# Optimization experiments

Measured on AMD Instinct MI355X. Metric: run time of the kernel, lower is better.

The kernel has to match this reference:

```python
import jax, jax.numpy as jnp
import numpy as np

K_DIM = 256
HEADS = 8


def setup_inputs() -> dict:
    key = jax.random.key(0)
    ks = jax.random.split(key, 6)
    b, t, k, h = 8, 1024, K_DIM, HEADS
    scale = 1.0 / np.sqrt(k)
    x = jax.random.normal(ks[0], (b, t, k), dtype=jnp.float32)
    # nn.Linear(k, k*h, bias=False) weights, stored as (in, out) for x @ W
    Wq = jax.random.normal(ks[1], (k, k * h), dtype=jnp.float32) * scale
    Wk = jax.random.normal(ks[2], (k, k * h), dtype=jnp.float32) * scale
    Wv = jax.random.normal(ks[3], (k, k * h), dtype=jnp.float32) * scale
    # unifyheads: nn.Linear(h*k, k) with bias
    Wu = jax.random.normal(ks[4], (h * k, k), dtype=jnp.float32) * (1.0 / np.sqrt(h * k))
    bu = jax.random.normal(ks[5], (k,), dtype=jnp.float32) * 0.01
    return {"x": x, "Wq": Wq, "Wk": Wk, "Wv": Wv, "Wu": Wu, "bu": bu}


def reference(x, Wq, Wk, Wv, Wu, bu):
    b, t, k = x.shape
    h = Wq.shape[1] // k
    inv4 = 1.0 / (k ** 0.25)  # scale Q and K each by k^(1/4) -> combined 1/sqrt(k)
    q = (x @ Wq).reshape(b, t, h, k) * inv4
    kk = (x @ Wk).reshape(b, t, h, k) * inv4
    v = (x @ Wv).reshape(b, t, h, k)
    # scores: [b, h, t, t]
    scores = jnp.einsum('bthk,bshk->bhts', q, kk)
    att = jax.nn.softmax(scores, axis=-1)
    out = jnp.einsum('bhts,bshk->bthk', att, v).reshape(b, t, h * k)
    return out @ Wu + bu
```

## Files before the change

### kernel.cpp

```cpp
#include <hip/hip_runtime.h>
#include <stdint.h>

typedef unsigned short u16;
typedef __attribute__((ext_vector_type(8))) short bf16x8;
typedef __attribute__((ext_vector_type(4))) float f32x4;

#define LOG2E 1.44269504088896340736f

__device__ __forceinline__ float bf2f(u16 u) {
  union { uint32_t u; float f; } v; v.u = ((uint32_t)u) << 16; return v.f;
}
__device__ __forceinline__ u16 f2bf(float f) {
  union { float f; uint32_t u; } v; v.f = f;
  uint32_t r = v.u + 0x7fffu + ((v.u >> 16) & 1u);
  return (u16)(r >> 16);
}

__device__ __forceinline__ void gl_lds16(const u16* g, u16* l) {
  __builtin_amdgcn_global_load_lds((const __attribute__((address_space(1))) void*)g,
                                   (__attribute__((address_space(3))) void*)l, 16, 0, 0);
}

__global__ __launch_bounds__(256) void k_cvt_x(const float* __restrict__ x,
                                               u16* __restrict__ xb) {
  const int i = blockIdx.x * 256 + threadIdx.x;
  float4 v = ((const float4*)x)[i];
  ushort4 o;
  o.x = f2bf(v.x); o.y = f2bf(v.y); o.z = f2bf(v.z); o.w = f2bf(v.w);
  ((ushort4*)xb)[i] = o;
}

__device__ __forceinline__ void transpose64f(const float* src, int sstride,
                                             u16* dst, int dstride,
                                             float scale, u16* tile ) {
  const int tid = threadIdx.x;
  const int row = tid >> 3, seg = tid & 7;
#pragma unroll
  for (int p = 0; p < 2; ++p) {
    int rr = p * 32 + row;
    int rw = rr ^ (seg * 8);
    float4 a = *(const float4*)(src + rr * sstride + seg * 8);
    float4 b = *(const float4*)(src + rr * sstride + seg * 8 + 4);
    tile[(seg * 8 + 0) * 80 + rw] = f2bf(a.x * scale);
    tile[(seg * 8 + 1) * 80 + rw] = f2bf(a.y * scale);
    tile[(seg * 8 + 2) * 80 + rw] = f2bf(a.z * scale);
    tile[(seg * 8 + 3) * 80 + rw] = f2bf(a.w * scale);
    tile[(seg * 8 + 4) * 80 + rw] = f2bf(b.x * scale);
    tile[(seg * 8 + 5) * 80 + rw] = f2bf(b.y * scale);
    tile[(seg * 8 + 6) * 80 + rw] = f2bf(b.z * scale);
    tile[(seg * 8 + 7) * 80 + rw] = f2bf(b.w * scale);
  }
  __syncthreads();
#pragma unroll
  for (int p = 0; p < 2; ++p) {
    int rr = p * 32 + row;
    int sw = (seg ^ ((rr >> 3) & 7)) * 8;
    *(uint4*)(dst + rr * dstride + seg * 8) = *(uint4*)(tile + rr * 80 + sw);
  }
}

__device__ __forceinline__ void transpose64(const u16* src, int sstride,
                                            u16* dst, int dstride, u16* tile) {
  const int tid = threadIdx.x;
  const int row = tid >> 3, seg = tid & 7;
  union { uint4 u; u16 s[8]; } tv;
#pragma unroll
  for (int p = 0; p < 2; ++p) {
    int rr = p * 32 + row;
    int rw = rr ^ (seg * 8);
    tv.u = *(const uint4*)(src + rr * sstride + seg * 8);
#pragma unroll
    for (int j = 0; j < 8; ++j)
      tile[(seg * 8 + j) * 80 + rw] = tv.s[j];
  }
  __syncthreads();
#pragma unroll
  for (int p = 0; p < 2; ++p) {
    int rr = p * 32 + row;
    int sw = (seg ^ ((rr >> 3) & 7)) * 8;
    *(uint4*)(dst + rr * dstride + seg * 8) = *(uint4*)(tile + rr * 80 + sw);
  }
}

__global__ __launch_bounds__(256) void k_transpose_wqkv(const float* __restrict__ Wq,
                                                        const float* __restrict__ Wk,
                                                        const float* __restrict__ Wv,
                                                        u16* __restrict__ Wt) {
  __shared__ u16 tile[64 * 80];
  const int o0 = blockIdx.x * 64, i0 = blockIdx.y * 64;
  const float* src; float scale = 0.25f; int oc0 = o0;
  if (o0 < 2048)      { src = Wq; }
  else if (o0 < 4096) { src = Wk; oc0 = o0 - 2048; }
  else                { src = Wv; oc0 = o0 - 4096; scale = 1.0f; }
  transpose64f(src + i0 * 2048 + oc0, 2048, Wt + o0 * 256 + i0, 256, scale, tile);
}

__global__ __launch_bounds__(256) void k_transpose_wu(const float* __restrict__ Wu,
                                                      u16* __restrict__ Wut) {
  __shared__ u16 tile[64 * 80];
  const int c0 = blockIdx.x * 64, r0 = blockIdx.y * 64;
  transpose64f(Wu + r0 * 256 + c0, 256, Wut + c0 * 2048 + r0, 2048, 1.0f, tile);
}

__global__ __launch_bounds__(256) void k_transpose_v(const u16* __restrict__ qkv,
                                                     u16* __restrict__ vt) {
  __shared__ u16 tile[64 * 80];
  const int bh = blockIdx.z;
  const int b = bh >> 3, h = bh & 7;
  const int t0 = blockIdx.y * 64, d0 = blockIdx.x * 64;
  const u16* src = qkv + ((size_t)(b * 1024 + t0)) * 6144 + 4096 + h * 256 + d0;
  u16* dst = vt + ((size_t)(bh * 256 + d0)) * 1024 + t0;
  transpose64(src, 6144, dst, 1024, tile);
}

__global__ __launch_bounds__(256) void k_gemm_qkv(const u16* __restrict__ A,
                                                  const u16* __restrict__ Bt,
                                                  u16* __restrict__ C) {
  __shared__ u16 As[128 * 32];
  __shared__ u16 Bs[128 * 32];
  const int m0 = blockIdx.y * 128, n0 = blockIdx.x * 128;
  const int tid = threadIdx.x, w = tid >> 6, lane = tid & 63;
  const int q = lane >> 4, r = lane & 15;
  const int wm = (w >> 1) * 64, wn = (w & 1) * 64;
  const int bo0 = w * 2048 + lane * 16;
  const int row0 = bo0 >> 6, col0 = (bo0 & 63) >> 1;
  const int bo1 = bo0 + 1024;
  const int row1 = bo1 >> 6, col1 = (bo1 & 63) >> 1;
  f32x4 acc[4][4] = {};
  for (int kt = 0; kt < 256; kt += 32) {
    __syncthreads();
    gl_lds16(A + (m0 + row0) * 256 + kt + col0, As + w * 1024);
    gl_lds16(A + (m0 + row1) * 256 + kt + col1, As + w * 1024 + 512);
    gl_lds16(Bt + (n0 + row0) * 256 + kt + col0, Bs + w * 1024);
    gl_lds16(Bt + (n0 + row1) * 256 + kt + col1, Bs + w * 1024 + 512);
    __syncthreads();
    bf16x8 af[4], bf[4];
#pragma unroll
    for (int mb = 0; mb < 4; ++mb) af[mb] = *(const bf16x8*)(As + (wm + mb * 16 + r) * 32 + q * 8);
#pragma unroll
    for (int nb = 0; nb < 4; ++nb) bf[nb] = *(const bf16x8*)(Bs + (wn + nb * 16 + r) * 32 + q * 8);
#pragma unroll
    for (int mb = 0; mb < 4; ++mb)
#pragma unroll
      for (int nb = 0; nb < 4; ++nb)
        acc[mb][nb] = __builtin_amdgcn_mfma_f32_16x16x32_bf16(af[mb], bf[nb], acc[mb][nb], 0, 0, 0);
  }
#pragma unroll
  for (int mb = 0; mb < 4; ++mb)
#pragma unroll
    for (int nb = 0; nb < 4; ++nb) {
      const int nn = n0 + wn + nb * 16 + r;
#pragma unroll
      for (int reg = 0; reg < 4; ++reg) {
        const int mm = m0 + wm + mb * 16 + q * 4 + reg;
        C[(size_t)mm * 6144 + nn] = f2bf(acc[mb][nb][reg]);
      }
    }
}

__global__ __launch_bounds__(256) void k_attn(const u16* __restrict__ qkv,
                                              const u16* __restrict__ vt,
                                              u16* __restrict__ att) {
  __shared__ u16 smem[16896];
  const int blk = blockIdx.x;
  const int qt = blk >> 6, bh = blk & 63;
  const int b = bh >> 3, h = bh & 7;
  const int tid = threadIdx.x, w = tid >> 6, lane = tid & 63;
  const int q = lane >> 4, r = lane & 15;
  const int t0 = qt * 64 + w * 16;

  const u16* Qg = qkv + ((size_t)(b * 1024 + t0 + r)) * 6144 + h * 256;
  bf16x8 qf[8];
#pragma unroll
  for (int kc = 0; kc < 8; ++kc) qf[kc] = *(const bf16x8*)(Qg + kc * 32 + q * 8);

  float m_i = -3.0e38f, l_i = 0.0f;
  f32x4 o[16] = {};

  const u16* Kg = qkv + (size_t)b * 1024 * 6144 + 2048 + h * 256;
  const u16* Vg = vt + (size_t)(b * 8 + h) * 256 * 1024;

  const int kc_s = (tid & 31) >> 2, kq_s = tid & 3;
  const int db_s = tid >> 4, vr_s = tid & 15;

  for (int sc = 0; sc < 1024; sc += 32) {
    __syncthreads();
    {
      uint4 kv[4];
#pragma unroll
      for (int p = 0; p < 4; ++p) {
        int key = p * 8 + (tid >> 5);
        kv[p] = *(const uint4*)(Kg + (size_t)(sc + key) * 6144 + (tid & 31) * 8);
      }
#pragma unroll
      for (int p = 0; p < 4; ++p) {
        int key = p * 8 + (tid >> 5);
        int sb = key >> 4, kr = key & 15;
        int unit = (kc_s * 2 + sb) * 64 + kq_s * 16 + ((kr + kq_s) & 15);
        *(uint4*)(smem + unit * 8) = kv[p];
      }
    }
    {
      uint4 vv[4];
#pragma unroll
      for (int p = 0; p < 4; ++p)
        vv[p] = *(const uint4*)(Vg + (size_t)tid * 1024 + sc + p * 8);
#pragma unroll
      for (int p = 0; p < 4; ++p) {
        int unit = db_s * 64 + p * 16 + ((vr_s + p) & 15);
        *(uint4*)(smem + 8192 + unit * 8) = vv[p];
      }
    }
    __syncthreads();

    f32x4 s0 = {}, s1 = {};
#pragma unroll
    for (int kc = 0; kc < 8; ++kc) {
      bf16x8 k0 = *(const bf16x8*)(smem + ((kc * 2 + 0) * 64 + q * 16 + ((r + q) & 15)) * 8);
      bf16x8 k1 = *(const bf16x8*)(smem + ((kc * 2 + 1) * 64 + q * 16 + ((r + q) & 15)) * 8);
      s0 = __builtin_amdgcn_mfma_f32_16x16x32_bf16(k0, qf[kc], s0, 0, 0, 0);
      s1 = __builtin_amdgcn_mfma_f32_16x16x32_bf16(k1, qf[kc], s1, 0, 0, 0);
    }

    float vmax = fmaxf(fmaxf(fmaxf(s0[0], s0[1]), fmaxf(s0[2], s0[3])),
                       fmaxf(fmaxf(s1[0], s1[1]), fmaxf(s1[2], s1[3])));
    vmax = fmaxf(vmax, __shfl_xor(vmax, 16));
    vmax = fmaxf(vmax, __shfl_xor(vmax, 32));
    float mn = fmaxf(m_i, vmax);
    float al = exp2f((m_i - mn) * LOG2E);
    float pa[4], pb[4];
    float rs = 0.0f;
#pragma unroll
    for (int reg = 0; reg < 4; ++reg) {
      pa[reg] = exp2f((s0[reg] - mn) * LOG2E);
      pb[reg] = exp2f((s1[reg] - mn) * LOG2E);
      rs += pa[reg] + pb[reg];
    }
    rs += __shfl_xor(rs, 16);
    rs += __shfl_xor(rs, 32);
    l_i = l_i * al + rs;
    m_i = mn;
    if (__any(al < 0.99999f)) {
#pragma unroll
      for (int db = 0; db < 16; ++db) {
        f32x4 t = o[db];
#pragma unroll
        for (int reg = 0; reg < 4; ++reg) t[reg] *= al;
        o[db] = t;
      }
    }

    uint32_t pk[4];
#pragma unroll
    for (int reg = 0; reg < 4; ++reg)
      pk[reg] = (uint32_t)f2bf(pa[reg]) | ((uint32_t)f2bf(pb[reg]) << 16);
    const int srcA = ((q & 1) << 5) + r;
    const int srcB = srcA + 16;
    uint32_t tt[8];
#pragma unroll
    for (int reg = 0; reg < 4; ++reg) tt[reg] = (uint32_t)__shfl((int)pk[reg], srcA);
#pragma unroll
    for (int reg = 0; reg < 4; ++reg) tt[4 + reg] = (uint32_t)__shfl((int)pk[reg], srcB);
    union { bf16x8 v; u16 e[8]; } pf;
    const bool hi = (q >= 2);
#pragma unroll
    for (int j = 0; j < 8; ++j)
      pf.e[j] = hi ? (u16)(tt[j] >> 16) : (u16)(tt[j] & 0xffffu);

#pragma unroll
    for (int db = 0; db < 16; ++db) {
      bf16x8 vf = *(const bf16x8*)(smem + 8192 + (db * 64 + q * 16 + ((r + q) & 15)) * 8);
      o[db] = __builtin_amdgcn_mfma_f32_16x16x32_bf16(vf, pf.v, o[db], 0, 0, 0);
    }
  }

  float rl = 1.0f / l_i;
  __syncthreads();
  u16* Os = smem + w * 4224;
#pragma unroll
  for (int db = 0; db < 16; ++db) {
    uint32_t lo = (uint32_t)f2bf(o[db][0] * rl) | ((uint32_t)f2bf(o[db][1] * rl) << 16);
    uint32_t hi2 = (uint32_t)f2bf(o[db][2] * rl) | ((uint32_t)f2bf(o[db][3] * rl) << 16);
    uint2 val; val.x = lo; val.y = hi2;
    *(uint2*)(Os + r * 264 + db * 16 + q * 4) = val;
  }
  asm volatile("s_waitcnt lgkmcnt(0)" ::: "memory");
  u16* Ag = att + ((size_t)(b * 1024 + t0)) * 2048 + h * 256;
#pragma unroll
  for (int p = 0; p < 8; ++p) {
    int idx = (p * 64 + lane) * 8;
    int row = idx >> 8, col = idx & 255;
    *(uint4*)(Ag + (size_t)row * 2048 + col) = *(uint4*)(Os + row * 264 + col);
  }
}

__global__ __launch_bounds__(256) void k_gemm_out(const u16* __restrict__ A,
                                                  const u16* __restrict__ Bt,
                                                  const float* __restrict__ bu,
                                                  float* __restrict__ C) {
  __shared__ u16 As[128 * 32];
  __shared__ u16 Bs[64 * 32];
  const int m0 = blockIdx.y * 128, n0 = blockIdx.x * 64;
  const int tid = threadIdx.x, w = tid >> 6, lane = tid & 63;
  const int q = lane >> 4, r = lane & 15;
  const int wm = (w >> 1) * 64, wn = (w & 1) * 32;
  const int boA0 = w * 2048 + lane * 16;
  const int rA0 = boA0 >> 6, cA0 = (boA0 & 63) >> 1;
  const int boA1 = boA0 + 1024;
  const int rA1 = boA1 >> 6, cA1 = (boA1 & 63) >> 1;
  const int boB = w * 1024 + lane * 16;
  const int rB = boB >> 6, cB = (boB & 63) >> 1;
  f32x4 acc[4][2] = {};
  for (int kt = 0; kt < 2048; kt += 32) {
    __syncthreads();
    gl_lds16(A + (size_t)(m0 + rA0) * 2048 + kt + cA0, As + w * 1024);
    gl_lds16(A + (size_t)(m0 + rA1) * 2048 + kt + cA1, As + w * 1024 + 512);
    gl_lds16(Bt + (size_t)(n0 + rB) * 2048 + kt + cB, Bs + w * 512);
    __syncthreads();
    bf16x8 af[4], bf[2];
#pragma unroll
    for (int mb = 0; mb < 4; ++mb) af[mb] = *(const bf16x8*)(As + (wm + mb * 16 + r) * 32 + q * 8);
#pragma unroll
    for (int nb = 0; nb < 2; ++nb) bf[nb] = *(const bf16x8*)(Bs + (wn + nb * 16 + r) * 32 + q * 8);
#pragma unroll
    for (int mb = 0; mb < 4; ++mb)
#pragma unroll
      for (int nb = 0; nb < 2; ++nb)
        acc[mb][nb] = __builtin_amdgcn_mfma_f32_16x16x32_bf16(af[mb], bf[nb], acc[mb][nb], 0, 0, 0);
  }
  float bias[2];
#pragma unroll
  for (int nb = 0; nb < 2; ++nb) bias[nb] = bu[n0 + wn + nb * 16 + r];
#pragma unroll
  for (int mb = 0; mb < 4; ++mb)
#pragma unroll
    for (int nb = 0; nb < 2; ++nb) {
      const int nn = n0 + wn + nb * 16 + r;
#pragma unroll
      for (int reg = 0; reg < 4; ++reg) {
        const int mm = m0 + wm + mb * 16 + q * 4 + reg;
        C[(size_t)mm * 256 + nn] = acc[mb][nb][reg] + bias[nb];
      }
    }
}

extern "C" void kernel_launch(void* const* d_in, const int* in_sizes, int n_in,
                              void* d_out, int out_size, void* d_ws, size_t ws_size,
                              hipStream_t stream) {
  const float* x  = (const float*)d_in[0];
  const float* Wq = (const float*)d_in[1];
  const float* Wk = (const float*)d_in[2];
  const float* Wv = (const float*)d_in[3];
  const float* Wu = (const float*)d_in[4];
  const float* bu = (const float*)d_in[5];
  float* outp = (float*)d_out;

  char* ws = (char*)d_ws;
  u16* qkv   = (u16*)(ws);
  u16* vt    = (u16*)(ws + 100663296);
  u16* attb  = (u16*)(ws + 134217728);
  u16* wqkvt = (u16*)(ws + 167772160);
  u16* wut   = (u16*)(ws + 170917888);
  u16* xb    = (u16*)(ws + 171966464);
  (void)in_sizes; (void)n_in; (void)out_size; (void)ws_size;

  dim3 blk(256);
  k_cvt_x<<<dim3(2048), blk, 0, stream>>>(x, xb);
  k_transpose_wqkv<<<dim3(96, 4), blk, 0, stream>>>(Wq, Wk, Wv, wqkvt);
  k_transpose_wu<<<dim3(4, 32), blk, 0, stream>>>(Wu, wut);
  k_gemm_qkv<<<dim3(48, 64), blk, 0, stream>>>(xb, wqkvt, qkv);
  k_transpose_v<<<dim3(4, 16, 64), blk, 0, stream>>>(qkv, vt);
  k_attn<<<dim3(1024), blk, 0, stream>>>(qkv, vt, attb);
  k_gemm_out<<<dim3(4, 64), blk, 0, stream>>>(attb, wut, bu, outp);
}
```

Baseline: 323.1 us.

## Process two 16-row query tiles per wave in attention kernel

Each wave now handles 32 query rows (two independent 16-row tiles) instead of 16, so every K/V tile staged in shared memory feeds twice as many MFMAs. The grid is halved to 512 blocks of 128 queries each, which halves the global-to-LDS traffic for K and V per query. In exchange, register pressure roughly doubles (two output accumulator sets of 16 f32x4), and there are fewer blocks to spread across the GPU's compute units. The launch bound now requests 2 blocks per SIMD.

```diff
diff --git a/kernel.cpp b/kernel.cpp
--- a/kernel.cpp
+++ b/kernel.cpp
@@ -158,24 +158,28 @@
     }
 }
 
-__global__ __launch_bounds__(256) void k_attn(const u16* __restrict__ qkv,
-                                              const u16* __restrict__ vt,
-                                              u16* __restrict__ att) {
+__global__ __launch_bounds__(256, 2) void k_attn(const u16* __restrict__ qkv,
+                                                 const u16* __restrict__ vt,
+                                                 u16* __restrict__ att) {
   __shared__ u16 smem[16896];
   const int blk = blockIdx.x;
   const int qt = blk >> 6, bh = blk & 63;
   const int b = bh >> 3, h = bh & 7;
   const int tid = threadIdx.x, w = tid >> 6, lane = tid & 63;
   const int q = lane >> 4, r = lane & 15;
-  const int t0 = qt * 64 + w * 16;
-
-  const u16* Qg = qkv + ((size_t)(b * 1024 + t0 + r)) * 6144 + h * 256;
-  bf16x8 qf[8];
-#pragma unroll
-  for (int kc = 0; kc < 8; ++kc) qf[kc] = *(const bf16x8*)(Qg + kc * 32 + q * 8);
-
-  float m_i = -3.0e38f, l_i = 0.0f;
-  f32x4 o[16] = {};
+  const int t0 = qt * 128 + w * 32;
+
+  const u16* QgA = qkv + ((size_t)(b * 1024 + t0 + r)) * 6144 + h * 256;
+  const u16* QgB = QgA + (size_t)16 * 6144;
+  bf16x8 qfA[8], qfB[8];
+#pragma unroll
+  for (int kc = 0; kc < 8; ++kc) {
+    qfA[kc] = *(const bf16x8*)(QgA + kc * 32 + q * 8);
+    qfB[kc] = *(const bf16x8*)(QgB + kc * 32 + q * 8);
+  }
+
+  float mA = -3.0e38f, lA = 0.0f, mB = -3.0e38f, lB = 0.0f;
+  f32x4 oA[16] = {}, oB[16] = {};
 
   const u16* Kg = qkv + (size_t)b * 1024 * 6144 + 2048 + h * 256;
   const u16* Vg = vt + (size_t)(b * 8 + h) * 256 * 1024;
@@ -213,84 +217,133 @@
     }
     __syncthreads();
 
-    f32x4 s0 = {}, s1 = {};
+    f32x4 s0A = {}, s1A = {}, s0B = {}, s1B = {};
 #pragma unroll
     for (int kc = 0; kc < 8; ++kc) {
       bf16x8 k0 = *(const bf16x8*)(smem + ((kc * 2 + 0) * 64 + q * 16 + ((r + q) & 15)) * 8);
       bf16x8 k1 = *(const bf16x8*)(smem + ((kc * 2 + 1) * 64 + q * 16 + ((r + q) & 15)) * 8);
-      s0 = __builtin_amdgcn_mfma_f32_16x16x32_bf16(k0, qf[kc], s0, 0, 0, 0);
-      s1 = __builtin_amdgcn_mfma_f32_16x16x32_bf16(k1, qf[kc], s1, 0, 0, 0);
-    }
-
-    float vmax = fmaxf(fmaxf(fmaxf(s0[0], s0[1]), fmaxf(s0[2], s0[3])),
-                       fmaxf(fmaxf(s1[0], s1[1]), fmaxf(s1[2], s1[3])));
-    vmax = fmaxf(vmax, __shfl_xor(vmax, 16));
-    vmax = fmaxf(vmax, __shfl_xor(vmax, 32));
-    float mn = fmaxf(m_i, vmax);
-    float al = exp2f((m_i - mn) * LOG2E);
-    float pa[4], pb[4];
-    float rs = 0.0f;
-#pragma unroll
-    for (int reg = 0; reg < 4; ++reg) {
-      pa[reg] = exp2f((s0[reg] - mn) * LOG2E);
-      pb[reg] = exp2f((s1[reg] - mn) * LOG2E);
-      rs += pa[reg] + pb[reg];
-    }
-    rs += __shfl_xor(rs, 16);
-    rs += __shfl_xor(rs, 32);
-    l_i = l_i * al + rs;
-    m_i = mn;
-    if (__any(al < 0.99999f)) {
+      s0A = __builtin_amdgcn_mfma_f32_16x16x32_bf16(k0, qfA[kc], s0A, 0, 0, 0);
+      s1A = __builtin_amdgcn_mfma_f32_16x16x32_bf16(k1, qfA[kc], s1A, 0, 0, 0);
+      s0B = __builtin_amdgcn_mfma_f32_16x16x32_bf16(k0, qfB[kc], s0B, 0, 0, 0);
+      s1B = __builtin_amdgcn_mfma_f32_16x16x32_bf16(k1, qfB[kc], s1B, 0, 0, 0);
+    }
+
+    union { bf16x8 v; u16 e[8]; } pfA, pfB;
+    float alA, alB;
+    {
+      float vmax = fmaxf(fmaxf(fmaxf(s0A[0], s0A[1]), fmaxf(s0A[2], s0A[3])),
+                         fmaxf(fmaxf(s1A[0], s1A[1]), fmaxf(s1A[2], s1A[3])));
+      vmax = fmaxf(vmax, __shfl_xor(vmax, 16));
+      vmax = fmaxf(vmax, __shfl_xor(vmax, 32));
+      float mn = fmaxf(mA, vmax);
+      alA = exp2f((mA - mn) * LOG2E);
+      float pa[4], pb[4], rs = 0.0f;
+#pragma unroll
+      for (int reg = 0; reg < 4; ++reg) {
+        pa[reg] = exp2f((s0A[reg] - mn) * LOG2E);
+        pb[reg] = exp2f((s1A[reg] - mn) * LOG2E);
+        rs += pa[reg] + pb[reg];
+      }
+      rs += __shfl_xor(rs, 16); rs += __shfl_xor(rs, 32);
+      lA = lA * alA + rs; mA = mn;
+      uint32_t pk[4];
+#pragma unroll
+      for (int reg = 0; reg < 4; ++reg)
+        pk[reg] = (uint32_t)f2bf(pa[reg]) | ((uint32_t)f2bf(pb[reg]) << 16);
+      const int srcA = ((q & 1) << 5) + r, srcB = srcA + 16;
+      uint32_t tt[8];
+#pragma unroll
+      for (int reg = 0; reg < 4; ++reg) tt[reg] = (uint32_t)__shfl((int)pk[reg], srcA);
+#pragma unroll
+      for (int reg = 0; reg < 4; ++reg) tt[4 + reg] = (uint32_t)__shfl((int)pk[reg], srcB);
+      const bool hi = (q >= 2);
+#pragma unroll
+      for (int j = 0; j < 8; ++j)
+        pfA.e[j] = hi ? (u16)(tt[j] >> 16) : (u16)(tt[j] & 0xffffu);
+    }
+    {
+      float vmax = fmaxf(fmaxf(fmaxf(s0B[0], s0B[1]), fmaxf(s0B[2], s0B[3])),
+                         fmaxf(fmaxf(s1B[0], s1B[1]), fmaxf(s1B[2], s1B[3])));
+      vmax = fmaxf(vmax, __shfl_xor(vmax, 16));
+      vmax = fmaxf(vmax, __shfl_xor(vmax, 32));
+      float mn = fmaxf(mB, vmax);
+      alB = exp2f((mB - mn) * LOG2E);
+      float pa[4], pb[4], rs = 0.0f;
+#pragma unroll
+      for (int reg = 0; reg < 4; ++reg) {
+        pa[reg] = exp2f((s0B[reg] - mn) * LOG2E);
+        pb[reg] = exp2f((s1B[reg] - mn) * LOG2E);
+        rs += pa[reg] + pb[reg];
+      }
+      rs += __shfl_xor(rs, 16); rs += __shfl_xor(rs, 32);
+      lB = lB * alB + rs; mB = mn;
+      uint32_t pk[4];
+#pragma unroll
+      for (int reg = 0; reg < 4; ++reg)
+        pk[reg] = (uint32_t)f2bf(pa[reg]) | ((uint32_t)f2bf(pb[reg]) << 16);
+      const int srcA = ((q & 1) << 5) + r, srcB = srcA + 16;
+      uint32_t tt[8];
+#pragma unroll
+      for (int reg = 0; reg < 4; ++reg) tt[reg] = (uint32_t)__shfl((int)pk[reg], srcA);
+#pragma unroll
+      for (int reg = 0; reg < 4; ++reg) tt[4 + reg] = (uint32_t)__shfl((int)pk[reg], srcB);
+      const bool hi = (q >= 2);
+#pragma unroll
+      for (int j = 0; j < 8; ++j)
+        pfB.e[j] = hi ? (u16)(tt[j] >> 16) : (u16)(tt[j] & 0xffffu);
+    }
+
+    if (__any(alA < 0.99999f)) {
 #pragma unroll
       for (int db = 0; db < 16; ++db) {
-        f32x4 t = o[db];
-#pragma unroll
-        for (int reg = 0; reg < 4; ++reg) t[reg] *= al;
-        o[db] = t;
-      }
-    }
-
-    uint32_t pk[4];
-#pragma unroll
-    for (int reg = 0; reg < 4; ++reg)
-      pk[reg] = (uint32_t)f2bf(pa[reg]) | ((uint32_t)f2bf(pb[reg]) << 16);
-    const int srcA = ((q & 1) << 5) + r;
-    const int srcB = srcA + 16;
-    uint32_t tt[8];
-#pragma unroll
-    for (int reg = 0; reg < 4; ++reg) tt[reg] = (uint32_t)__shfl((int)pk[reg], srcA);
-#pragma unroll
-    for (int reg = 0; reg < 4; ++reg) tt[4 + reg] = (uint32_t)__shfl((int)pk[reg], srcB);
-    union { bf16x8 v; u16 e[8]; } pf;
-    const bool hi = (q >= 2);
-#pragma unroll
-    for (int j = 0; j < 8; ++j)
-      pf.e[j] = hi ? (u16)(tt[j] >> 16) : (u16)(tt[j] & 0xffffu);
+        f32x4 t = oA[db];
+#pragma unroll
+        for (int reg = 0; reg < 4; ++reg) t[reg] *= alA;
+        oA[db] = t;
+      }
+    }
+    if (__any(alB < 0.99999f)) {
+#pragma unroll
+      for (int db = 0; db < 16; ++db) {
+        f32x4 t = oB[db];
+#pragma unroll
+        for (int reg = 0; reg < 4; ++reg) t[reg] *= alB;
+        oB[db] = t;
+      }
+    }
 
 #pragma unroll
     for (int db = 0; db < 16; ++db) {
       bf16x8 vf = *(const bf16x8*)(smem + 8192 + (db * 64 + q * 16 + ((r + q) & 15)) * 8);
-      o[db] = __builtin_amdgcn_mfma_f32_16x16x32_bf16(vf, pf.v, o[db], 0, 0, 0);
-    }
-  }
-
-  float rl = 1.0f / l_i;
+      oA[db] = __builtin_amdgcn_mfma_f32_16x16x32_bf16(vf, pfA.v, oA[db], 0, 0, 0);
+      oB[db] = __builtin_amdgcn_mfma_f32_16x16x32_bf16(vf, pfB.v, oB[db], 0, 0, 0);
+    }
+  }
+
   __syncthreads();
   u16* Os = smem + w * 4224;
-#pragma unroll
-  for (int db = 0; db < 16; ++db) {
-    uint32_t lo = (uint32_t)f2bf(o[db][0] * rl) | ((uint32_t)f2bf(o[db][1] * rl) << 16);
-    uint32_t hi2 = (uint32_t)f2bf(o[db][2] * rl) | ((uint32_t)f2bf(o[db][3] * rl) << 16);
-    uint2 val; val.x = lo; val.y = hi2;
-    *(uint2*)(Os + r * 264 + db * 16 + q * 4) = val;
-  }
-  asm volatile("s_waitcnt lgkmcnt(0)" ::: "memory");
-  u16* Ag = att + ((size_t)(b * 1024 + t0)) * 2048 + h * 256;
-#pragma unroll
-  for (int p = 0; p < 8; ++p) {
-    int idx = (p * 64 + lane) * 8;
-    int row = idx >> 8, col = idx & 255;
-    *(uint4*)(Ag + (size_t)row * 2048 + col) = *(uint4*)(Os + row * 264 + col);
+  float rlA = 1.0f / lA, rlB = 1.0f / lB;
+#pragma unroll
+  for (int pass = 0; pass < 2; ++pass) {
+    const f32x4* o = pass ? oB : oA;
+    const float rl = pass ? rlB : rlA;
+    const int tb = t0 + pass * 16;
+    __syncthreads();
+#pragma unroll
+    for (int db = 0; db < 16; ++db) {
+      uint32_t lo = (uint32_t)f2bf(o[db][0] * rl) | ((uint32_t)f2bf(o[db][1] * rl) << 16);
+      uint32_t hi2 = (uint32_t)f2bf(o[db][2] * rl) | ((uint32_t)f2bf(o[db][3] * rl) << 16);
+      uint2 val; val.x = lo; val.y = hi2;
+      *(uint2*)(Os + r * 264 + db * 16 + q * 4) = val;
+    }
+    asm volatile("s_waitcnt lgkmcnt(0)" ::: "memory");
+    u16* Ag = att + ((size_t)(b * 1024 + tb)) * 2048 + h * 256;
+#pragma unroll
+    for (int p = 0; p < 8; ++p) {
+      int idx = (p * 64 + lane) * 8;
+      int row = idx >> 8, col = idx & 255;
+      *(uint4*)(Ag + (size_t)row * 2048 + col) = *(uint4*)(Os + row * 264 + col);
+    }
   }
 }
 
@@ -370,6 +423,6 @@
   k_transpose_wu<<<dim3(4, 32), blk, 0, stream>>>(Wu, wut);
   k_gemm_qkv<<<dim3(48, 64), blk, 0, stream>>>(xb, wqkvt, qkv);
   k_transpose_v<<<dim3(4, 16, 64), blk, 0, stream>>>(qkv, vt);
-  k_attn<<<dim3(1024), blk, 0, stream>>>(qkv, vt, attb);
+  k_attn<<<dim3(512), blk, 0, stream>>>(qkv, vt, attb);
   k_gemm_out<<<dim3(4, 64), blk, 0, stream>>>(attb, wut, bu, outp);
 }
```

After: 282.4 us. -12.6%, faster.
